# Kernel optimization log

Hardware: AMD Instinct MI355X
Metric: run time of the kernel (lower is better)

## Reference

```python
import jax, jax.numpy as jnp
import numpy as np

B, LQ, C = 4, 4096, 384
NH, NL, NP = 6, 1, 4
HL, WL = 64, 64
LV = HL * WL
DH = C // NH
EPS = 1e-6


def layer_norm(x, g, b):
    mu = jnp.mean(x, axis=-1, keepdims=True)
    var = jnp.mean(jnp.square(x - mu), axis=-1, keepdims=True)
    return (x - mu) * jax.lax.rsqrt(var + EPS) * g + b


def ms_deform_attn_core(value, spatial_shapes, level_start_index, loc, attn_w):
    # value [B,LV,NH,DH]; loc [B,LQ,NH,NL,NP,2] in [0,1]; attn_w [B,LQ,NH,NL,NP]
    ss = np.asarray(spatial_shapes)
    lsi = np.asarray(level_start_index)
    Bv, _, nH, dh = value.shape
    Lq = loc.shape[1]
    nP = loc.shape[4]
    out = jnp.zeros((Bv, Lq, nH, dh), value.dtype)
    for l in range(loc.shape[3]):
        Hl, Wl = int(ss[l, 0]), int(ss[l, 1])
        st = int(lsi[l])
        vflat = value[:, st:st + Hl * Wl]  # [B, Hl*Wl, nH, dh]
        xy = loc[:, :, :, l]               # [B,LQ,nH,NP,2]
        # grid_sample(align_corners=False): pixel = loc * size - 0.5
        x = xy[..., 0] * Wl - 0.5
        y = xy[..., 1] * Hl - 0.5
        x0 = jnp.floor(x)
        y0 = jnp.floor(y)
        wx = x - x0
        wy = y - y0
        x0i = x0.astype(jnp.int32)
        y0i = y0.astype(jnp.int32)

        def gather(xi, yi):
            # zero padding outside the feature map (padding_mode='zeros')
            valid = (xi >= 0) & (xi < Wl) & (yi >= 0) & (yi < Hl)
            idx = jnp.clip(yi, 0, Hl - 1) * Wl + jnp.clip(xi, 0, Wl - 1)  # [B,LQ,nH,NP]
            idx2 = idx.transpose(0, 1, 3, 2).reshape(Bv, Lq * nP, nH)
            g = jnp.take_along_axis(vflat, idx2[..., None], axis=1)       # [B,LQ*NP,nH,dh]
            g = g.reshape(Bv, Lq, nP, nH, dh).transpose(0, 1, 3, 2, 4)    # [B,LQ,nH,NP,dh]
            return g * valid[..., None].astype(value.dtype)

        samp = (gather(x0i, y0i) * ((1 - wx) * (1 - wy))[..., None]
                + gather(x0i + 1, y0i) * (wx * (1 - wy))[..., None]
                + gather(x0i, y0i + 1) * ((1 - wx) * wy)[..., None]
                + gather(x0i + 1, y0i + 1) * (wx * wy)[..., None])
        out = out + jnp.einsum('bqhpd,bqhp->bqhd', samp, attn_w[:, :, :, l])
    return out.reshape(Bv, Lq, nH * dh)


def setup_inputs() -> dict:
    key = jax.random.key(0)
    ks = jax.random.split(key, 12)
    s = 0.02
    return {
        'query': jax.random.normal(ks[0], (B, LQ, C), jnp.float32),
        'reference_points': jax.random.uniform(ks[1], (B, LQ, NL, 2), dtype=jnp.float32),
        'feat': jax.random.normal(ks[2], (B, LV, C), jnp.float32),
        'spatial_shapes': jnp.array([[HL, WL]], jnp.int32),
        'level_start_index': jnp.array([0], jnp.int32),
        'ln_q_g': jnp.ones((C,), jnp.float32), 'ln_q_b': jnp.zeros((C,), jnp.float32),
        'ln_f_g': jnp.ones((C,), jnp.float32), 'ln_f_b': jnp.zeros((C,), jnp.float32),
        'gamma': jax.random.normal(ks[3], (C,), jnp.float32) * 0.1,
        'Wv': jax.random.normal(ks[4], (C, C), jnp.float32) * s,
        'bv': jnp.zeros((C,), jnp.float32),
        'Wo': jax.random.normal(ks[5], (C, NH * NL * NP * 2), jnp.float32) * s,
        'bo': jax.random.normal(ks[6], (NH * NL * NP * 2,), jnp.float32) * 0.5,
        'Wa': jax.random.normal(ks[7], (C, NH * NL * NP), jnp.float32) * s,
        'ba': jnp.zeros((NH * NL * NP,), jnp.float32),
        'Wout': jax.random.normal(ks[8], (C, C), jnp.float32) * s,
        'bout': jnp.zeros((C,), jnp.float32),
    }


def reference(query, reference_points, feat, spatial_shapes, level_start_index,
              ln_q_g, ln_q_b, ln_f_g, ln_f_b, gamma,
              Wv, bv, Wo, bo, Wa, ba, Wout, bout):
    q = layer_norm(query, ln_q_g, ln_q_b)
    f = layer_norm(feat, ln_f_g, ln_f_b)
    value = (f @ Wv + bv).reshape(B, LV, NH, DH)
    offsets = (q @ Wo + bo).reshape(B, LQ, NH, NL, NP, 2)
    attn_w = jax.nn.softmax((q @ Wa + ba).reshape(B, LQ, NH, NL * NP), axis=-1)
    attn_w = attn_w.reshape(B, LQ, NH, NL, NP)
    # offset normalizer is (W, H) per level
    norm = jnp.stack([spatial_shapes[:, 1], spatial_shapes[:, 0]], -1).astype(jnp.float32)
    loc = reference_points[:, :, None, :, None, :] + offsets / norm[None, None, None, :, None, :]
    attn = ms_deform_attn_core(value, spatial_shapes, level_start_index, loc, attn_w)
    attn = attn @ Wout + bout
    return query + gamma * attn
```

## Files before the change

kernel.cpp:

```cpp
#include <hip/hip_runtime.h>
#include <math.h>

#define B_    4
#define LQ_   4096
#define C_    384
#define NH_   6
#define NP_   4
#define HL_   64
#define WL_   64
#define LV_   (HL_ * WL_)
#define ROWS_ (B_ * LQ_)
#define EPS_  1e-6f
#define NOFF_ 48
#define NLOG_ 24

typedef unsigned short u16;
typedef unsigned int   u32;
typedef __bf16 bf16x8 __attribute__((ext_vector_type(8)));
typedef float  f32x4  __attribute__((ext_vector_type(4)));

__device__ __forceinline__ u16 f2bf(float f) {
    u32 u = __float_as_uint(f);
    u += 0x7fff + ((u >> 16) & 1);
    return (u16)(u >> 16);
}
__device__ __forceinline__ u32 pack2bf(float a, float b) {
    return (u32)f2bf(a) | ((u32)f2bf(b) << 16);
}

__device__ __forceinline__ f32x4 mfma16(bf16x8 a, bf16x8 b, f32x4 c) {
    return __builtin_amdgcn_mfma_f32_16x16x32_bf16(a, b, c, 0, 0, 0);
}

__device__ __forceinline__ void gl_lds16(const u16* g, u16* l) {
    __builtin_amdgcn_global_load_lds(
        (const __attribute__((address_space(1))) unsigned int*)g,
        (__attribute__((address_space(3))) unsigned int*)l, 16, 0, 0);
}

#define LN_BLOCKS_   8192
#define PREP_BLOCKS_ 1273

__global__ __launch_bounds__(256) void ln_prep(
    const float* __restrict__ query, const float* __restrict__ feat,
    const float* __restrict__ qg, const float* __restrict__ qbv,
    const float* __restrict__ fg, const float* __restrict__ fbv,
    u16* __restrict__ qout, u16* __restrict__ fout,
    const float* __restrict__ Wv, const float* __restrict__ Wout,
    const float* __restrict__ Wo, const float* __restrict__ Wa,
    const float* __restrict__ bo, const float* __restrict__ ba,
    u16* __restrict__ WvT, u16* __restrict__ WoutT, u16* __restrict__ WcT,
    float* __restrict__ bias_c)
{
    if (blockIdx.x < LN_BLOCKS_) {
        int wid  = threadIdx.x >> 6;
        int lane = threadIdx.x & 63;
        int row  = blockIdx.x * 4 + wid;
        const float *src, *g, *bsh;
        u16* dst;
        int r;
        if (row < ROWS_) { src = query; g = qg; bsh = qbv; dst = qout; r = row; }
        else             { src = feat;  g = fg; bsh = fbv; dst = fout; r = row - ROWS_; }

        const float* x = src + (size_t)r * C_;
        float4 a4 = *(const float4*)(x + 4 * lane);
        float2 a2 = *(const float2*)(x + 256 + 2 * lane);
        float v0 = a4.x, v1 = a4.y, v2 = a4.z, v3 = a4.w, v4 = a2.x, v5 = a2.y;

        float s = v0 + v1 + v2 + v3 + v4 + v5;
#pragma unroll
        for (int off = 32; off; off >>= 1) s += __shfl_xor(s, off);
        float mu = s * (1.f / C_);

        float d0 = v0 - mu, d1 = v1 - mu, d2 = v2 - mu;
        float d3 = v3 - mu, d4 = v4 - mu, d5 = v5 - mu;
        float s2 = d0*d0 + d1*d1 + d2*d2 + d3*d3 + d4*d4 + d5*d5;
#pragma unroll
        for (int off = 32; off; off >>= 1) s2 += __shfl_xor(s2, off);
        float rs = rsqrtf(s2 * (1.f / C_) + EPS_);

        float4 g4 = *(const float4*)(g + 4 * lane);
        float4 b4 = *(const float4*)(bsh + 4 * lane);
        float2 g2 = *(const float2*)(g + 256 + 2 * lane);
        float2 b2 = *(const float2*)(bsh + 256 + 2 * lane);

        float o0 = d0 * rs * g4.x + b4.x;
        float o1 = d1 * rs * g4.y + b4.y;
        float o2 = d2 * rs * g4.z + b4.z;
        float o3 = d3 * rs * g4.w + b4.w;
        float o4 = d4 * rs * g2.x + b2.x;
        float o5 = d5 * rs * g2.y + b2.y;

        u16* y = dst + (size_t)r * C_;
        uint2 w0; w0.x = pack2bf(o0, o1); w0.y = pack2bf(o2, o3);
        *(uint2*)(y + 4 * lane) = w0;
        *(u32*)(y + 256 + 2 * lane) = pack2bf(o4, o5);
    } else {
        const int KN = 384 * 384;
        int idx = (blockIdx.x - LN_BLOCKS_) * 256 + threadIdx.x;
        if (idx < KN) {
            int n = idx / 384, k = idx - n * 384;
            WvT[idx] = f2bf(Wv[k * 384 + n]);
        } else if (idx < 2 * KN) {
            int t = idx - KN;
            int n = t / 384, k = t - n * 384;
            WoutT[t] = f2bf(Wout[k * 384 + n]);
        } else if (idx < 2 * KN + 80 * 384) {
            int t = idx - 2 * KN;
            int n = t / 384, k = t - n * 384;
            float v = (n < 48) ? Wo[k * 48 + n] : (n < 72 ? Wa[k * 24 + (n - 48)] : 0.f);
            WcT[t] = f2bf(v);
        } else if (idx < 2 * KN + 80 * 384 + 80) {
            int n = idx - (2 * KN + 80 * 384);
            bias_c[n] = (n < 48) ? bo[n] : (n < 72 ? ba[n - 48] : 0.f);
        }
    }
}

__global__ __launch_bounds__(256) void gemm_combined(
    const u16* __restrict__ fb, const u16* __restrict__ qb,
    const u16* __restrict__ WvT, const u16* __restrict__ WcT,
    const float* __restrict__ bv, const float* __restrict__ bias_c,
    u16* __restrict__ valb, float* __restrict__ offs, float* __restrict__ logits)
{
    const int K = 384;
    __shared__ __align__(16) u16 As[128 * 32];
    __shared__ __align__(16) u16 Bs[128 * 32];

    int g    = blockIdx.x;
    int tid  = threadIdx.x;
    int lane = tid & 63, wid = tid >> 6;
    int fr = lane & 15, quad = lane >> 4;

    int srow = tid >> 2;
    int scol = (tid & 3) * 8;

    if (g < 384) {
        int m0 = (g & 127) * 128, n0 = (g >> 7) * 128;
        const u16* agp0 = fb  + (size_t)(m0 + srow) * K + scol;
        const u16* agp1 = fb  + (size_t)(m0 + 64 + srow) * K + scol;
        const u16* bgp0 = WvT + (size_t)(n0 + srow) * K + scol;
        const u16* bgp1 = WvT + (size_t)(n0 + 64 + srow) * K + scol;
        u16* al0 = As + tid * 8;  u16* al1 = As + 2048 + tid * 8;
        u16* bl0 = Bs + tid * 8;  u16* bl1 = Bs + 2048 + tid * 8;

        int wm = (wid >> 1) * 64, wn = (wid & 1) * 64;

        f32x4 zero = {0.f, 0.f, 0.f, 0.f};
        f32x4 acc[4][4];
#pragma unroll
        for (int i = 0; i < 4; ++i)
#pragma unroll
            for (int j = 0; j < 4; ++j) acc[i][j] = zero;

        for (int k0 = 0; k0 < K; k0 += 32) {
            gl_lds16(agp0 + k0, al0);
            gl_lds16(agp1 + k0, al1);
            gl_lds16(bgp0 + k0, bl0);
            gl_lds16(bgp1 + k0, bl1);
            __syncthreads();
            bf16x8 af[4], bfr[4];
#pragma unroll
            for (int i = 0; i < 4; ++i)
                af[i] = *(bf16x8*)&As[(wm + i * 16 + fr) * 32 + quad * 8];
#pragma unroll
            for (int j = 0; j < 4; ++j)
                bfr[j] = *(bf16x8*)&Bs[(wn + j * 16 + fr) * 32 + quad * 8];
#pragma unroll
            for (int i = 0; i < 4; ++i)
#pragma unroll
                for (int j = 0; j < 4; ++j)
                    acc[i][j] = mfma16(af[i], bfr[j], acc[i][j]);
            __syncthreads();
        }

#pragma unroll
        for (int i = 0; i < 4; ++i) {
            int row = m0 + wm + i * 16 + quad * 4;
#pragma unroll
            for (int j = 0; j < 4; ++j) {
                int col = n0 + wn + j * 16 + fr;
                float bcol = bv[col];
#pragma unroll
                for (int r = 0; r < 4; ++r)
                    valb[(size_t)(row + r) * C_ + col] = f2bf(acc[i][j][r] + bcol);
            }
        }
    } else {
        int m0 = (g - 384) * 128;
        const u16* agp0 = qb + (size_t)(m0 + srow) * K + scol;
        const u16* agp1 = qb + (size_t)(m0 + 64 + srow) * K + scol;
        u16* al0 = As + tid * 8;  u16* al1 = As + 2048 + tid * 8;
        const u16* bgp0 = WcT + (size_t)srow * K + scol;
        const u16* bgp1 = WcT + (size_t)(64 + srow) * K + scol;
        u16* bl0 = Bs + tid * 8;
        u16* bl1 = Bs + 2048 + tid * 8;

        int wm = wid * 32;

        f32x4 zero = {0.f, 0.f, 0.f, 0.f};
        f32x4 acc[2][5];
#pragma unroll
        for (int i = 0; i < 2; ++i)
#pragma unroll
            for (int j = 0; j < 5; ++j) acc[i][j] = zero;

        for (int k0 = 0; k0 < K; k0 += 32) {
            gl_lds16(agp0 + k0, al0);
            gl_lds16(agp1 + k0, al1);
            gl_lds16(bgp0 + k0, bl0);
            if (tid < 64) gl_lds16(bgp1 + k0, bl1);
            __syncthreads();
            bf16x8 af[2], bfr[5];
#pragma unroll
            for (int i = 0; i < 2; ++i)
                af[i] = *(bf16x8*)&As[(wm + i * 16 + fr) * 32 + quad * 8];
#pragma unroll
            for (int j = 0; j < 5; ++j)
                bfr[j] = *(bf16x8*)&Bs[(j * 16 + fr) * 32 + quad * 8];
#pragma unroll
            for (int i = 0; i < 2; ++i)
#pragma unroll
                for (int j = 0; j < 5; ++j)
                    acc[i][j] = mfma16(af[i], bfr[j], acc[i][j]);
            __syncthreads();
        }

#pragma unroll
        for (int i = 0; i < 2; ++i) {
            int row = m0 + wm + i * 16 + quad * 4;
#pragma unroll
            for (int j = 0; j < 5; ++j) {
                int col = j * 16 + fr;
                if (col < 72) {
                    float bcol = bias_c[col];
#pragma unroll
                    for (int r = 0; r < 4; ++r) {
                        float v = acc[i][j][r] + bcol;
                        if (col < 48) offs[(size_t)(row + r) * NOFF_ + col] = v;
                        else          logits[(size_t)(row + r) * NLOG_ + (col - 48)] = v;
                    }
                }
            }
        }
    }
}

__global__ __launch_bounds__(384) void sampler(
    const u16*  __restrict__ value,
    const float* __restrict__ rp,
    const float* __restrict__ offs,
    const float* __restrict__ logits,
    u16* __restrict__ attn)
{
    int t = threadIdx.x;
    int g = blockIdx.x;
    int b     = (g & 7) >> 1;
    int local = ((g >> 3) << 1) | (g & 1);
    int q  = t / 48, dc = t - q * 48;
    int h  = dc >> 3;
    int col0 = dc << 3;
    int r  = b * LQ_ + local * 8 + q;

    float4 lg  = *(const float4*)(logits + (size_t)r * NLOG_ + h * 4);
    float2 rpv = *(const float2*)(rp + (size_t)r * 2);
    float4 of0 = *(const float4*)(offs + (size_t)r * NOFF_ + h * 8);
    float4 of1 = *(const float4*)(offs + (size_t)r * NOFF_ + h * 8 + 4);

    float mx = fmaxf(fmaxf(lg.x, lg.y), fmaxf(lg.z, lg.w));
    float e0 = __expf(lg.x - mx), e1 = __expf(lg.y - mx);
    float e2 = __expf(lg.z - mx), e3 = __expf(lg.w - mx);
    float rden = 1.f / (e0 + e1 + e2 + e3);
    float aws[4] = {e0 * rden, e1 * rden, e2 * rden, e3 * rden};
    float oxs[4] = {of0.x, of0.z, of1.x, of1.z};
    float oys[4] = {of0.y, of0.w, of1.y, of1.w};

    const u16* vbase = value + (size_t)b * LV_ * C_ + col0;
    float acc[8] = {0.f, 0.f, 0.f, 0.f, 0.f, 0.f, 0.f, 0.f};
#pragma unroll
    for (int p = 0; p < NP_; ++p) {
        float x = rpv.x * (float)WL_ + oxs[p] - 0.5f;
        float y = rpv.y * (float)HL_ + oys[p] - 0.5f;
        float x0f = floorf(x), y0f = floorf(y);
        float wx = x - x0f, wy = y - y0f;
        int x0 = (int)x0f, y0 = (int)y0f;
#pragma unroll
        for (int c = 0; c < 4; ++c) {
            int xi = x0 + (c & 1);
            int yi = y0 + (c >> 1);
            bool valid = (xi >= 0) && (xi < WL_) && (yi >= 0) && (yi < HL_);
            int xc = xi < 0 ? 0 : (xi > WL_ - 1 ? WL_ - 1 : xi);
            int yc = yi < 0 ? 0 : (yi > HL_ - 1 ? HL_ - 1 : yi);
            float w = ((c & 1) ? wx : 1.f - wx) * ((c >> 1) ? wy : 1.f - wy) * aws[p];
            w = valid ? w : 0.f;
            bf16x8 vv = *(const bf16x8*)(vbase + (size_t)(yc * WL_ + xc) * C_);
#pragma unroll
            for (int e = 0; e < 8; ++e) acc[e] += w * (float)vv[e];
        }
    }

    uint4 o;
    o.x = pack2bf(acc[0], acc[1]);
    o.y = pack2bf(acc[2], acc[3]);
    o.z = pack2bf(acc[4], acc[5]);
    o.w = pack2bf(acc[6], acc[7]);
    *(uint4*)(attn + (size_t)r * C_ + col0) = o;
}

__global__ __launch_bounds__(256) void out_gemm(
    const u16* __restrict__ A, const u16* __restrict__ Bt,
    const float* __restrict__ bout, const float* __restrict__ gamma,
    const float* __restrict__ query, float* __restrict__ out)
{
    const int K = 384;
    __shared__ __align__(16) u16 As[128 * 32];
    __shared__ __align__(16) u16 Bs[128 * 32];

    int g    = blockIdx.x;
    int tid  = threadIdx.x;
    int lane = tid & 63, wid = tid >> 6;
    int fr = lane & 15, quad = lane >> 4;

    int srow = tid >> 2;
    int scol = (tid & 3) * 8;

    int m0 = (g & 127) * 128, n0 = (g >> 7) * 128;
    const u16* agp0 = A  + (size_t)(m0 + srow) * K + scol;
    const u16* agp1 = A  + (size_t)(m0 + 64 + srow) * K + scol;
    const u16* bgp0 = Bt + (size_t)(n0 + srow) * K + scol;
    const u16* bgp1 = Bt + (size_t)(n0 + 64 + srow) * K + scol;
    u16* al0 = As + tid * 8;  u16* al1 = As + 2048 + tid * 8;
    u16* bl0 = Bs + tid * 8;  u16* bl1 = Bs + 2048 + tid * 8;

    int wm = (wid >> 1) * 64, wn = (wid & 1) * 64;

    f32x4 zero = {0.f, 0.f, 0.f, 0.f};
    f32x4 acc[4][4];
#pragma unroll
    for (int i = 0; i < 4; ++i)
#pragma unroll
        for (int j = 0; j < 4; ++j) acc[i][j] = zero;

    for (int k0 = 0; k0 < K; k0 += 32) {
        gl_lds16(agp0 + k0, al0);
        gl_lds16(agp1 + k0, al1);
        gl_lds16(bgp0 + k0, bl0);
        gl_lds16(bgp1 + k0, bl1);
        __syncthreads();
        bf16x8 af[4], bfr[4];
#pragma unroll
        for (int i = 0; i < 4; ++i)
            af[i] = *(bf16x8*)&As[(wm + i * 16 + fr) * 32 + quad * 8];
#pragma unroll
        for (int j = 0; j < 4; ++j)
            bfr[j] = *(bf16x8*)&Bs[(wn + j * 16 + fr) * 32 + quad * 8];
#pragma unroll
        for (int i = 0; i < 4; ++i)
#pragma unroll
            for (int j = 0; j < 4; ++j)
                acc[i][j] = mfma16(af[i], bfr[j], acc[i][j]);
        __syncthreads();
    }

#pragma unroll
    for (int i = 0; i < 4; ++i) {
        int row = m0 + wm + i * 16 + quad * 4;
#pragma unroll
        for (int j = 0; j < 4; ++j) {
            int col = n0 + wn + j * 16 + fr;
            float bc = bout[col], gm = gamma[col];
#pragma unroll
            for (int r = 0; r < 4; ++r) {
                size_t o = (size_t)(row + r) * C_ + col;
                out[o] = query[o] + gm * (acc[i][j][r] + bc);
            }
        }
    }
}

extern "C" void kernel_launch(void* const* d_in, const int* in_sizes, int n_in,
                              void* d_out, int out_size, void* d_ws, size_t ws_size,
                              hipStream_t stream)
{
    const float* query  = (const float*)d_in[0];
    const float* rp     = (const float*)d_in[1];
    const float* feat   = (const float*)d_in[2];
    const float* gamma  = (const float*)d_in[9];
    const float* Wv     = (const float*)d_in[10];
    const float* bv     = (const float*)d_in[11];
    const float* Wo     = (const float*)d_in[12];
    const float* bo     = (const float*)d_in[13];
    const float* Wa     = (const float*)d_in[14];
    const float* ba     = (const float*)d_in[15];
    const float* Wout   = (const float*)d_in[16];
    const float* bout   = (const float*)d_in[17];
    float* out = (float*)d_out;

    u16* wsu    = (u16*)d_ws;
    u16* qb     = wsu;
    u16* fb     = qb    + (size_t)ROWS_ * C_;
    u16* valb   = fb    + (size_t)ROWS_ * C_;
    u16* attnb  = valb  + (size_t)ROWS_ * C_;
    u16* WvT    = attnb + (size_t)ROWS_ * C_;
    u16* WoutT  = WvT   + 384 * 384;
    u16* WcT    = WoutT + 384 * 384;
    float* offs   = (float*)(WcT + 80 * 384);
    float* logits = offs + (size_t)ROWS_ * NOFF_;
    float* bias_c = logits + (size_t)ROWS_ * NLOG_;

    ln_prep<<<LN_BLOCKS_ + PREP_BLOCKS_, 256, 0, stream>>>(
        query, feat,
        (const float*)d_in[5], (const float*)d_in[6],
        (const float*)d_in[7], (const float*)d_in[8],
        qb, fb, Wv, Wout, Wo, Wa, bo, ba, WvT, WoutT, WcT, bias_c);

    gemm_combined<<<512, 256, 0, stream>>>(fb, qb, WvT, WcT, bv, bias_c,
                                           valb, offs, logits);

    sampler<<<2048, 384, 0, stream>>>(valb, rp, offs, logits, attnb);

    out_gemm<<<384, 256, 0, stream>>>(attnb, WoutT, bout, gamma, query, out);
}
```

Before: 169.8 us.

## Fuse layer norm into projection GEMM prologue and drop bf16 intermediates

The standalone layer-norm pass over query and feat is removed. Each GEMM block now computes per-row mean and rsqrt variance from the fp32 input. It then normalizes and converts the A tile to bf16 in registers before storing it to LDS, while weight tiles still use global-to-LDS loads. This removes the bf16 qb/fb round trip and one kernel's worth of traffic. In exchange, the fp32 rows are re-read by every column tile and again in the stats pass, the A loads become synchronous register loads, and the variance is computed as E[x²]−mu².

```diff
diff --git a/kernel.cpp b/kernel.cpp
--- a/kernel.cpp
+++ b/kernel.cpp
@@ -38,87 +38,37 @@
         (__attribute__((address_space(3))) unsigned int*)l, 16, 0, 0);
 }
 
-#define LN_BLOCKS_   8192
-#define PREP_BLOCKS_ 1273
-
-__global__ __launch_bounds__(256) void ln_prep(
-    const float* __restrict__ query, const float* __restrict__ feat,
-    const float* __restrict__ qg, const float* __restrict__ qbv,
-    const float* __restrict__ fg, const float* __restrict__ fbv,
-    u16* __restrict__ qout, u16* __restrict__ fout,
+__global__ __launch_bounds__(256) void prep_weights(
     const float* __restrict__ Wv, const float* __restrict__ Wout,
     const float* __restrict__ Wo, const float* __restrict__ Wa,
     const float* __restrict__ bo, const float* __restrict__ ba,
     u16* __restrict__ WvT, u16* __restrict__ WoutT, u16* __restrict__ WcT,
     float* __restrict__ bias_c)
 {
-    if (blockIdx.x < LN_BLOCKS_) {
-        int wid  = threadIdx.x >> 6;
-        int lane = threadIdx.x & 63;
-        int row  = blockIdx.x * 4 + wid;
-        const float *src, *g, *bsh;
-        u16* dst;
-        int r;
-        if (row < ROWS_) { src = query; g = qg; bsh = qbv; dst = qout; r = row; }
-        else             { src = feat;  g = fg; bsh = fbv; dst = fout; r = row - ROWS_; }
-
-        const float* x = src + (size_t)r * C_;
-        float4 a4 = *(const float4*)(x + 4 * lane);
-        float2 a2 = *(const float2*)(x + 256 + 2 * lane);
-        float v0 = a4.x, v1 = a4.y, v2 = a4.z, v3 = a4.w, v4 = a2.x, v5 = a2.y;
-
-        float s = v0 + v1 + v2 + v3 + v4 + v5;
-#pragma unroll
-        for (int off = 32; off; off >>= 1) s += __shfl_xor(s, off);
-        float mu = s * (1.f / C_);
-
-        float d0 = v0 - mu, d1 = v1 - mu, d2 = v2 - mu;
-        float d3 = v3 - mu, d4 = v4 - mu, d5 = v5 - mu;
-        float s2 = d0*d0 + d1*d1 + d2*d2 + d3*d3 + d4*d4 + d5*d5;
-#pragma unroll
-        for (int off = 32; off; off >>= 1) s2 += __shfl_xor(s2, off);
-        float rs = rsqrtf(s2 * (1.f / C_) + EPS_);
-
-        float4 g4 = *(const float4*)(g + 4 * lane);
-        float4 b4 = *(const float4*)(bsh + 4 * lane);
-        float2 g2 = *(const float2*)(g + 256 + 2 * lane);
-        float2 b2 = *(const float2*)(bsh + 256 + 2 * lane);
-
-        float o0 = d0 * rs * g4.x + b4.x;
-        float o1 = d1 * rs * g4.y + b4.y;
-        float o2 = d2 * rs * g4.z + b4.z;
-        float o3 = d3 * rs * g4.w + b4.w;
-        float o4 = d4 * rs * g2.x + b2.x;
-        float o5 = d5 * rs * g2.y + b2.y;
-
-        u16* y = dst + (size_t)r * C_;
-        uint2 w0; w0.x = pack2bf(o0, o1); w0.y = pack2bf(o2, o3);
-        *(uint2*)(y + 4 * lane) = w0;
-        *(u32*)(y + 256 + 2 * lane) = pack2bf(o4, o5);
-    } else {
-        const int KN = 384 * 384;
-        int idx = (blockIdx.x - LN_BLOCKS_) * 256 + threadIdx.x;
-        if (idx < KN) {
-            int n = idx / 384, k = idx - n * 384;
-            WvT[idx] = f2bf(Wv[k * 384 + n]);
-        } else if (idx < 2 * KN) {
-            int t = idx - KN;
-            int n = t / 384, k = t - n * 384;
-            WoutT[t] = f2bf(Wout[k * 384 + n]);
-        } else if (idx < 2 * KN + 80 * 384) {
-            int t = idx - 2 * KN;
-            int n = t / 384, k = t - n * 384;
-            float v = (n < 48) ? Wo[k * 48 + n] : (n < 72 ? Wa[k * 24 + (n - 48)] : 0.f);
-            WcT[t] = f2bf(v);
-        } else if (idx < 2 * KN + 80 * 384 + 80) {
-            int n = idx - (2 * KN + 80 * 384);
-            bias_c[n] = (n < 48) ? bo[n] : (n < 72 ? ba[n - 48] : 0.f);
-        }
-    }
-}
-
-__global__ __launch_bounds__(256) void gemm_combined(
-    const u16* __restrict__ fb, const u16* __restrict__ qb,
+    const int KN = 384 * 384;
+    int idx = blockIdx.x * 256 + threadIdx.x;
+    if (idx < KN) {
+        int n = idx / 384, k = idx - n * 384;
+        WvT[idx] = f2bf(Wv[k * 384 + n]);
+    } else if (idx < 2 * KN) {
+        int t = idx - KN;
+        int n = t / 384, k = t - n * 384;
+        WoutT[t] = f2bf(Wout[k * 384 + n]);
+    } else if (idx < 2 * KN + 80 * 384) {
+        int t = idx - 2 * KN;
+        int n = t / 384, k = t - n * 384;
+        float v = (n < 48) ? Wo[k * 48 + n] : (n < 72 ? Wa[k * 24 + (n - 48)] : 0.f);
+        WcT[t] = f2bf(v);
+    } else if (idx < 2 * KN + 80 * 384 + 80) {
+        int n = idx - (2 * KN + 80 * 384);
+        bias_c[n] = (n < 48) ? bo[n] : (n < 72 ? ba[n - 48] : 0.f);
+    }
+}
+
+__global__ __launch_bounds__(256) void gemm_ln(
+    const float* __restrict__ feat, const float* __restrict__ query,
+    const float* __restrict__ fg, const float* __restrict__ fbv,
+    const float* __restrict__ qg, const float* __restrict__ qbv,
     const u16* __restrict__ WvT, const u16* __restrict__ WcT,
     const float* __restrict__ bv, const float* __restrict__ bias_c,
     u16* __restrict__ valb, float* __restrict__ offs, float* __restrict__ logits)
@@ -126,24 +76,61 @@
     const int K = 384;
     __shared__ __align__(16) u16 As[128 * 32];
     __shared__ __align__(16) u16 Bs[128 * 32];
+    __shared__ float lng[384], lnb[384];
+    __shared__ float mu_s[128], rs_s[128];
 
     int g    = blockIdx.x;
     int tid  = threadIdx.x;
     int lane = tid & 63, wid = tid >> 6;
     int fr = lane & 15, quad = lane >> 4;
-
     int srow = tid >> 2;
     int scol = (tid & 3) * 8;
 
-    if (g < 384) {
-        int m0 = (g & 127) * 128, n0 = (g >> 7) * 128;
-        const u16* agp0 = fb  + (size_t)(m0 + srow) * K + scol;
-        const u16* agp1 = fb  + (size_t)(m0 + 64 + srow) * K + scol;
+    bool value_path = (g < 384);
+    const float* A  = value_path ? feat : query;
+    const float* gg = value_path ? fg   : qg;
+    const float* bb = value_path ? fbv  : qbv;
+    int m0 = value_path ? (g & 127) * 128 : (g - 384) * 128;
+    int n0 = value_path ? (g >> 7) * 128 : 0;
+
+    for (int i = tid; i < 384; i += 256) { lng[i] = gg[i]; lnb[i] = bb[i]; }
+
+    for (int i0 = 0; i0 < 32; i0 += 4) {
+        float4 a4[4]; float2 a2[4];
+#pragma unroll
+        for (int r = 0; r < 4; ++r) {
+            const float* x = A + (size_t)(m0 + wid * 32 + i0 + r) * C_;
+            a4[r] = *(const float4*)(x + 4 * lane);
+            a2[r] = *(const float2*)(x + 256 + 2 * lane);
+        }
+#pragma unroll
+        for (int r = 0; r < 4; ++r) {
+            float s  = a4[r].x + a4[r].y + a4[r].z + a4[r].w + a2[r].x + a2[r].y;
+            float s2 = a4[r].x * a4[r].x + a4[r].y * a4[r].y + a4[r].z * a4[r].z
+                     + a4[r].w * a4[r].w + a2[r].x * a2[r].x + a2[r].y * a2[r].y;
+#pragma unroll
+            for (int off = 32; off; off >>= 1) {
+                s  += __shfl_xor(s, off);
+                s2 += __shfl_xor(s2, off);
+            }
+            if (lane == 0) {
+                float mu  = s * (1.f / C_);
+                float var = s2 * (1.f / C_) - mu * mu;
+                mu_s[wid * 32 + i0 + r] = mu;
+                rs_s[wid * 32 + i0 + r] = rsqrtf(var + EPS_);
+            }
+        }
+    }
+    __syncthreads();
+
+    float mu0 = mu_s[srow],      rs0 = rs_s[srow];
+    float mu1 = mu_s[srow + 64], rs1 = rs_s[srow + 64];
+    const float* ar0 = A + (size_t)(m0 + srow) * C_ + scol;
+    const float* ar1 = A + (size_t)(m0 + 64 + srow) * C_ + scol;
+
+    if (value_path) {
         const u16* bgp0 = WvT + (size_t)(n0 + srow) * K + scol;
         const u16* bgp1 = WvT + (size_t)(n0 + 64 + srow) * K + scol;
-        u16* al0 = As + tid * 8;  u16* al1 = As + 2048 + tid * 8;
-        u16* bl0 = Bs + tid * 8;  u16* bl1 = Bs + 2048 + tid * 8;
-
         int wm = (wid >> 1) * 64, wn = (wid & 1) * 64;
 
         f32x4 zero = {0.f, 0.f, 0.f, 0.f};
@@ -154,10 +141,27 @@
             for (int j = 0; j < 4; ++j) acc[i][j] = zero;
 
         for (int k0 = 0; k0 < K; k0 += 32) {
-            gl_lds16(agp0 + k0, al0);
-            gl_lds16(agp1 + k0, al1);
-            gl_lds16(bgp0 + k0, bl0);
-            gl_lds16(bgp1 + k0, bl1);
+            gl_lds16(bgp0 + k0, Bs + tid * 8);
+            gl_lds16(bgp1 + k0, Bs + 2048 + tid * 8);
+            float4 u0 = *(const float4*)(ar0 + k0);
+            float4 u1 = *(const float4*)(ar0 + k0 + 4);
+            float4 v0 = *(const float4*)(ar1 + k0);
+            float4 v1 = *(const float4*)(ar1 + k0 + 4);
+            float4 g0 = *(const float4*)&lng[k0 + scol];
+            float4 g1 = *(const float4*)&lng[k0 + scol + 4];
+            float4 b0 = *(const float4*)&lnb[k0 + scol];
+            float4 b1 = *(const float4*)&lnb[k0 + scol + 4];
+            uint4 w0, w1;
+            w0.x = pack2bf((u0.x - mu0) * rs0 * g0.x + b0.x, (u0.y - mu0) * rs0 * g0.y + b0.y);
+            w0.y = pack2bf((u0.z - mu0) * rs0 * g0.z + b0.z, (u0.w - mu0) * rs0 * g0.w + b0.w);
+            w0.z = pack2bf((u1.x - mu0) * rs0 * g1.x + b1.x, (u1.y - mu0) * rs0 * g1.y + b1.y);
+            w0.w = pack2bf((u1.z - mu0) * rs0 * g1.z + b1.z, (u1.w - mu0) * rs0 * g1.w + b1.w);
+            w1.x = pack2bf((v0.x - mu1) * rs1 * g0.x + b0.x, (v0.y - mu1) * rs1 * g0.y + b0.y);
+            w1.y = pack2bf((v0.z - mu1) * rs1 * g0.z + b0.z, (v0.w - mu1) * rs1 * g0.w + b0.w);
+            w1.z = pack2bf((v1.x - mu1) * rs1 * g1.x + b1.x, (v1.y - mu1) * rs1 * g1.y + b1.y);
+            w1.w = pack2bf((v1.z - mu1) * rs1 * g1.z + b1.z, (v1.w - mu1) * rs1 * g1.w + b1.w);
+            *(uint4*)(As + tid * 8)        = w0;
+            *(uint4*)(As + 2048 + tid * 8) = w1;
             __syncthreads();
             bf16x8 af[4], bfr[4];
 #pragma unroll
@@ -187,15 +191,8 @@
             }
         }
     } else {
-        int m0 = (g - 384) * 128;
-        const u16* agp0 = qb + (size_t)(m0 + srow) * K + scol;
-        const u16* agp1 = qb + (size_t)(m0 + 64 + srow) * K + scol;
-        u16* al0 = As + tid * 8;  u16* al1 = As + 2048 + tid * 8;
         const u16* bgp0 = WcT + (size_t)srow * K + scol;
         const u16* bgp1 = WcT + (size_t)(64 + srow) * K + scol;
-        u16* bl0 = Bs + tid * 8;
-        u16* bl1 = Bs + 2048 + tid * 8;
-
         int wm = wid * 32;
 
         f32x4 zero = {0.f, 0.f, 0.f, 0.f};
@@ -206,10 +203,27 @@
             for (int j = 0; j < 5; ++j) acc[i][j] = zero;
 
         for (int k0 = 0; k0 < K; k0 += 32) {
-            gl_lds16(agp0 + k0, al0);
-            gl_lds16(agp1 + k0, al1);
-            gl_lds16(bgp0 + k0, bl0);
-            if (tid < 64) gl_lds16(bgp1 + k0, bl1);
+            gl_lds16(bgp0 + k0, Bs + tid * 8);
+            if (tid < 64) gl_lds16(bgp1 + k0, Bs + 2048 + tid * 8);
+            float4 u0 = *(const float4*)(ar0 + k0);
+            float4 u1 = *(const float4*)(ar0 + k0 + 4);
+            float4 v0 = *(const float4*)(ar1 + k0);
+            float4 v1 = *(const float4*)(ar1 + k0 + 4);
+            float4 g0 = *(const float4*)&lng[k0 + scol];
+            float4 g1 = *(const float4*)&lng[k0 + scol + 4];
+            float4 b0 = *(const float4*)&lnb[k0 + scol];
+            float4 b1 = *(const float4*)&lnb[k0 + scol + 4];
+            uint4 w0, w1;
+            w0.x = pack2bf((u0.x - mu0) * rs0 * g0.x + b0.x, (u0.y - mu0) * rs0 * g0.y + b0.y);
+            w0.y = pack2bf((u0.z - mu0) * rs0 * g0.z + b0.z, (u0.w - mu0) * rs0 * g0.w + b0.w);
+            w0.z = pack2bf((u1.x - mu0) * rs0 * g1.x + b1.x, (u1.y - mu0) * rs0 * g1.y + b1.y);
+            w0.w = pack2bf((u1.z - mu0) * rs0 * g1.z + b1.z, (u1.w - mu0) * rs0 * g1.w + b1.w);
+            w1.x = pack2bf((v0.x - mu1) * rs1 * g0.x + b0.x, (v0.y - mu1) * rs1 * g0.y + b0.y);
+            w1.y = pack2bf((v0.z - mu1) * rs1 * g0.z + b0.z, (v0.w - mu1) * rs1 * g0.w + b0.w);
+            w1.z = pack2bf((v1.x - mu1) * rs1 * g1.x + b1.x, (v1.y - mu1) * rs1 * g1.y + b1.y);
+            w1.w = pack2bf((v1.z - mu1) * rs1 * g1.z + b1.z, (v1.w - mu1) * rs1 * g1.w + b1.w);
+            *(uint4*)(As + tid * 8)        = w0;
+            *(uint4*)(As + 2048 + tid * 8) = w1;
             __syncthreads();
             bf16x8 af[2], bfr[5];
 #pragma unroll
@@ -397,9 +411,7 @@
     float* out = (float*)d_out;
 
     u16* wsu    = (u16*)d_ws;
-    u16* qb     = wsu;
-    u16* fb     = qb    + (size_t)ROWS_ * C_;
-    u16* valb   = fb    + (size_t)ROWS_ * C_;
+    u16* valb   = wsu;
     u16* attnb  = valb  + (size_t)ROWS_ * C_;
     u16* WvT    = attnb + (size_t)ROWS_ * C_;
     u16* WoutT  = WvT   + 384 * 384;
@@ -408,14 +420,13 @@
     float* logits = offs + (size_t)ROWS_ * NOFF_;
     float* bias_c = logits + (size_t)ROWS_ * NLOG_;
 
-    ln_prep<<<LN_BLOCKS_ + PREP_BLOCKS_, 256, 0, stream>>>(
-        query, feat,
+    prep_weights<<<1273, 256, 0, stream>>>(Wv, Wout, Wo, Wa, bo, ba,
+                                           WvT, WoutT, WcT, bias_c);
+
+    gemm_ln<<<512, 256, 0, stream>>>(feat, query,
+        (const float*)d_in[7], (const float*)d_in[8],
         (const float*)d_in[5], (const float*)d_in[6],
-        (const float*)d_in[7], (const float*)d_in[8],
-        qb, fb, Wv, Wout, Wo, Wa, bo, ba, WvT, WoutT, WcT, bias_c);
-
-    gemm_combined<<<512, 256, 0, stream>>>(fb, qb, WvT, WcT, bv, bias_c,
-                                           valb, offs, logits);
+        WvT, WcT, bv, bias_c, valb, offs, logits);
 
     sampler<<<2048, 384, 0, stream>>>(valb, rp, offs, logits, attnb);
 
```

New measurement: 180.6 us. +6.4%, slower.
